# Kernel tuning notes

Measured on AMD Instinct MI355X. Metric: run time of the kernel, lower is better.

Reference implementation:

```python
import jax, jax.numpy as jnp
import numpy as np

THETA = 10000.0


def _apply_rope(xh, positions, theta):
    # xh: [B, H, S, d_k]; positions: [S] int
    d_k = xh.shape[-1]
    inv_freq = theta ** (-jnp.arange(0, d_k, 2, dtype=jnp.float32) / d_k)  # [d_k/2]
    angles = positions.astype(jnp.float32)[:, None] * inv_freq[None, :]     # [S, d_k/2]
    cos = jnp.cos(angles)
    sin = jnp.sin(angles)
    x1 = xh[..., 0::2]
    x2 = xh[..., 1::2]
    r1 = x1 * cos - x2 * sin
    r2 = x1 * sin + x2 * cos
    return jnp.stack([r1, r2], axis=-1).reshape(xh.shape)


def setup_inputs() -> dict:
    key = jax.random.key(0)
    ks = jax.random.split(key, 5)
    B, S, D = 2, 2048, 1024
    std = np.sqrt(1.0 / D).astype(np.float32)
    return {
        "x": jax.random.normal(ks[0], (B, S, D), dtype=jnp.float32),
        "token_positions": jnp.arange(S, dtype=jnp.int64 if jax.config.jax_enable_x64 else jnp.int32),
        "Wq": jax.random.normal(ks[1], (D, D), dtype=jnp.float32) * std,
        "Wk": jax.random.normal(ks[2], (D, D), dtype=jnp.float32) * std,
        "Wv": jax.random.normal(ks[3], (D, D), dtype=jnp.float32) * std,
        "Wo": jax.random.normal(ks[4], (D, D), dtype=jnp.float32) * std,
    }


def reference(x, token_positions, Wq, Wk, Wv, Wo):
    B, S, D = x.shape
    n_heads = 16
    d_k = D // n_heads

    # QKV projections (torch does x @ W.T)
    q = x @ Wq.T
    k = x @ Wk.T
    v = x @ Wv.T

    def split_heads(t):  # [B,S,D] -> [B,H,S,d_k]
        return t.reshape(B, S, n_heads, d_k).transpose(0, 2, 1, 3)

    qh = _apply_rope(split_heads(q), token_positions, THETA)
    kh = _apply_rope(split_heads(k), token_positions, THETA)
    vh = split_heads(v)

    scores = jnp.einsum("bhqd,bhkd->bhqk", qh, kh) / jnp.sqrt(jnp.float32(d_k))
    causal = jnp.tril(jnp.ones((S, S), dtype=bool))
    scores = jnp.where(causal, scores, -jnp.inf)
    attn = jax.nn.softmax(scores, axis=-1)

    out_h = jnp.einsum("bhqk,bhkd->bhqd", attn, vh)  # [B,H,S,d_k]
    out = out_h.transpose(0, 2, 1, 3).reshape(B, S, D)
    return out @ Wo.T
```

## Files before the change

### kernel.cpp

```cpp
#include <hip/hip_runtime.h>

typedef unsigned int u32;
typedef __attribute__((ext_vector_type(8))) short short8;
typedef __attribute__((ext_vector_type(4))) float f32x4;

__device__ __forceinline__ unsigned short f2bf(float f) {
  union { float f; u32 u; } x; x.f = f;
  u32 u = x.u;
  return (unsigned short)((u + 0x7fffu + ((u >> 16) & 1u)) >> 16);
}
__device__ __forceinline__ float bf2f(unsigned short b) {
  union { u32 u; float f; } x; x.u = ((u32)b) << 16;
  return x.f;
}
__device__ __forceinline__ f32x4 mfma_bf16(short8 a, short8 b, f32x4 c) {
  return __builtin_amdgcn_mfma_f32_16x16x32_bf16(a, b, c, 0, 0, 0);
}

typedef __attribute__((address_space(3))) unsigned int lds_u32;
typedef const __attribute__((address_space(1))) unsigned int glb_u32;
__device__ __forceinline__ void gload_lds16(const unsigned short* g, unsigned short* l) {
  __builtin_amdgcn_global_load_lds((glb_u32*)g, (lds_u32*)l, 16, 0, 0);
}

__global__ __launch_bounds__(256) void cvt_kernel(const float* __restrict__ src,
                                                  unsigned short* __restrict__ dst, int n4) {
  int i = blockIdx.x * 256 + threadIdx.x;
  if (i >= n4) return;
  float4 v = ((const float4*)src)[i];
  ushort4 o;
  o.x = f2bf(v.x); o.y = f2bf(v.y); o.z = f2bf(v.z); o.w = f2bf(v.w);
  ((ushort4*)dst)[i] = o;
}

__global__ __launch_bounds__(256) void cvt_w_kernel(const float* __restrict__ wq,
                                                    const float* __restrict__ wk,
                                                    const float* __restrict__ wv,
                                                    const float* __restrict__ wo,
                                                    unsigned short* __restrict__ dqkv,
                                                    unsigned short* __restrict__ dwo) {
  const int i = blockIdx.x * 256 + threadIdx.x;
  const int w = blockIdx.y;
  const float* src = (w == 0) ? wq : (w == 1) ? wk : (w == 2) ? wv : wo;
  unsigned short* dst = (w == 3) ? dwo : dqkv + (size_t)w * 1048576;
  float4 v = ((const float4*)src)[i];
  ushort4 o;
  o.x = f2bf(v.x); o.y = f2bf(v.y); o.z = f2bf(v.z); o.w = f2bf(v.w);
  ((ushort4*)dst)[i] = o;
}

__global__ __launch_bounds__(256) void gemm_qkv(const unsigned short* __restrict__ A,
                                                const unsigned short* __restrict__ B,
                                                unsigned short* __restrict__ qk,
                                                unsigned short* __restrict__ kk,
                                                unsigned short* __restrict__ vtm) {
  constexpr int K = 1024;
  __shared__ unsigned short As[128 * 32];
  __shared__ unsigned short Bs[128 * 32];
  const int tid = threadIdx.x;
  const int wave = tid >> 6, lane = tid & 63;
  const int l15 = lane & 15, quad = lane >> 4;
  const int wr = wave >> 1, wc = wave & 1;
  const int m0 = blockIdx.y * 128, n0 = blockIdx.x * 128;
  f32x4 acc[4][4] = {};
  const int srow = wave * 32 + (lane >> 2);
  const int scol = (lane & 3) * 8;
  const unsigned short* Ag0 = A + (size_t)(m0 + srow) * K + scol;
  const unsigned short* Ag1 = A + (size_t)(m0 + srow + 16) * K + scol;
  const unsigned short* Bg0 = B + (size_t)(n0 + srow) * K + scol;
  const unsigned short* Bg1 = B + (size_t)(n0 + srow + 16) * K + scol;
  unsigned short* Al0 = &As[wave * 1024];
  unsigned short* Al1 = &As[wave * 1024 + 512];
  unsigned short* Bl0 = &Bs[wave * 1024];
  unsigned short* Bl1 = &Bs[wave * 1024 + 512];
  for (int k0 = 0; k0 < K; k0 += 32) {
    __syncthreads();
    gload_lds16(Ag0 + k0, Al0);
    gload_lds16(Ag1 + k0, Al1);
    gload_lds16(Bg0 + k0, Bl0);
    gload_lds16(Bg1 + k0, Bl1);
    __syncthreads();
    short8 a[4], b[4];
#pragma unroll
    for (int i = 0; i < 4; ++i) a[i] = *(const short8*)&As[(wr * 64 + i * 16 + l15) * 32 + quad * 8];
#pragma unroll
    for (int j = 0; j < 4; ++j) b[j] = *(const short8*)&Bs[(wc * 64 + j * 16 + l15) * 32 + quad * 8];
#pragma unroll
    for (int i = 0; i < 4; ++i)
#pragma unroll
      for (int j = 0; j < 4; ++j) acc[i][j] = mfma_bf16(a[i], b[j], acc[i][j]);
  }
  const int proj = n0 >> 10;
  const int nn0 = (n0 & 1023) + wc * 64;
  if (proj < 2) {
    unsigned short* dst = (proj == 0) ? qk : kk;
#pragma unroll
    for (int i = 0; i < 4; ++i) {
      const int mb = m0 + wr * 64 + i * 16 + quad * 4;
#pragma unroll
      for (int j = 0; j < 4; ++j) {
        const int nn = nn0 + j * 16 + l15;
#pragma unroll
        for (int r = 0; r < 4; ++r) dst[(size_t)(mb + r) * 1024 + nn] = f2bf(acc[i][j][r]);
      }
    }
  } else {
#pragma unroll
    for (int i = 0; i < 4; ++i) {
      const int mb = m0 + wr * 64 + i * 16 + quad * 4;
      const int bb = mb >> 11, s = mb & 2047;
#pragma unroll
      for (int j = 0; j < 4; ++j) {
        const int nn = nn0 + j * 16 + l15;
        const int h = nn >> 6, d = nn & 63;
        ushort4 v4;
        v4.x = f2bf(acc[i][j][0]); v4.y = f2bf(acc[i][j][1]);
        v4.z = f2bf(acc[i][j][2]); v4.w = f2bf(acc[i][j][3]);
        *(ushort4*)&vtm[(((size_t)bb * 16 + h) * 64 + d) * 2048 + s] = v4;
      }
    }
  }
}

__global__ __launch_bounds__(256) void rope_kernel(unsigned short* __restrict__ q,
                                                   unsigned short* __restrict__ k,
                                                   const int* __restrict__ pos) {
  const int idx = blockIdx.x * 256 + threadIdx.x;
  const int i = idx & 31;
  const int h = (idx >> 5) & 15;
  const int s = (idx >> 9) & 2047;
  const int b = idx >> 20;
  const float p = (float)pos[s];
  const float inv = exp2f(-0.4152410118609203f * (float)i);
  float sn, cs;
  sincosf(p * inv, &sn, &cs);
  const size_t base = ((size_t)(b * 2048 + s)) * 1024 + h * 64 + 2 * i;
  {
    u32* qp = (u32*)(q + base);
    u32 w = *qp;
    float x1 = bf2f((unsigned short)(w & 0xffff)), x2 = bf2f((unsigned short)(w >> 16));
    *qp = (u32)f2bf(x1 * cs - x2 * sn) | ((u32)f2bf(x1 * sn + x2 * cs) << 16);
  }
  {
    u32* kp = (u32*)(k + base);
    u32 w = *kp;
    float x1 = bf2f((unsigned short)(w & 0xffff)), x2 = bf2f((unsigned short)(w >> 16));
    *kp = (u32)f2bf(x1 * cs - x2 * sn) | ((u32)f2bf(x1 * sn + x2 * cs) << 16);
  }
}

__global__ __launch_bounds__(256) void attn_shared(const unsigned short* __restrict__ qk,
                                                   const unsigned short* __restrict__ kk,
                                                   const unsigned short* __restrict__ vtm,
                                                   unsigned short* __restrict__ om) {
  __shared__ unsigned short Ks[64 * 64];
  __shared__ unsigned short Vs[64 * 64];
  __shared__ u32 PTb[4][2][16 * 36];
  const int tid = threadIdx.x;
  const int wave = tid >> 6, lane = tid & 63;
  const int l15 = lane & 15, quad = lane >> 4;
  u32* PT0 = &PTb[wave][0][0];
  u32* PT1 = &PTb[wave][1][0];
  const int bid = blockIdx.x;
  const int bh = bid & 31;
  const int qblk = 15 - (bid >> 5);
  const int b = bh >> 4, h = bh & 15;
  const int qbase = qblk * 128 + wave * 32;
  const unsigned short* Qp = qk + (size_t)b * 2048 * 1024 + h * 64;
  const unsigned short* Kp = kk + (size_t)b * 2048 * 1024 + h * 64;
  const unsigned short* Vp = vtm + (size_t)bh * 64 * 2048;
  short8 qf[2][2];
#pragma unroll
  for (int f = 0; f < 2; ++f)
#pragma unroll
    for (int hh = 0; hh < 2; ++hh)
      qf[f][hh] = *(const short8*)(Qp + (size_t)(qbase + f * 16 + l15) * 1024 + hh * 32 + quad * 8);
  f32x4 o4[2][4] = {};
  f32x4 ls[2] = {};
  short8 ones;
#pragma unroll
  for (int j = 0; j < 8; ++j) ones[j] = (short)0x3F80;
  const float SC = 0.18033688011112042f;
  const int nkb = (qblk * 128 + 191) >> 6;
  const int nkw = (qbase + 95) >> 6;
  const int srow = wave * 16 + (lane >> 3);
  const int scs = (((lane & 7) ^ (srow & 7)) * 8);
  const unsigned short* KgB = Kp + (size_t)srow * 1024 + scs;
  const unsigned short* VgB = Vp + (size_t)srow * 2048 + scs;
  unsigned short* Kl0 = &Ks[(wave * 16) * 64];
  unsigned short* Kl1 = &Ks[(wave * 16 + 8) * 64];
  unsigned short* Vl0 = &Vs[(wave * 16) * 64];
  unsigned short* Vl1 = &Vs[(wave * 16 + 8) * 64];
  const int sw0 = ((quad ^ (l15 & 7)) * 8);
  const int sw1 = (((4 + quad) ^ (l15 & 7)) * 8);
  for (int kt = 0; kt < nkb; ++kt) {
    const int kbase = kt << 6;
    __syncthreads();
    gload_lds16(KgB + (size_t)kbase * 1024, Kl0);
    gload_lds16(KgB + (size_t)kbase * 1024 + 8 * 1024, Kl1);
    gload_lds16(VgB + kbase, Vl0);
    gload_lds16(VgB + kbase + 8 * 2048, Vl1);
    __syncthreads();
    if (kt < nkw) {
      short8 kb[4][2], vb[4][2];
#pragma unroll
      for (int nt = 0; nt < 4; ++nt) {
        kb[nt][0] = *(const short8*)&Ks[(nt * 16 + l15) * 64 + sw0];
        kb[nt][1] = *(const short8*)&Ks[(nt * 16 + l15) * 64 + sw1];
      }
#pragma unroll
      for (int t = 0; t < 4; ++t) {
        vb[t][0] = *(const short8*)&Vs[(t * 16 + l15) * 64 + sw0];
        vb[t][1] = *(const short8*)&Vs[(t * 16 + l15) * 64 + sw1];
      }
      f32x4 s4[2][4] = {};
#pragma unroll
      for (int f = 0; f < 2; ++f)
#pragma unroll
        for (int nt = 0; nt < 4; ++nt) {
          s4[f][nt] = mfma_bf16(kb[nt][0], qf[f][0], s4[f][nt]);
          s4[f][nt] = mfma_bf16(kb[nt][1], qf[f][1], s4[f][nt]);
        }
      const bool edge = (kbase + 63 > qbase);
#pragma unroll
      for (int f = 0; f < 2; ++f) {
        const int qrow = qbase + f * 16 + l15;
        u32* PTf = f ? PT1 : PT0;
#pragma unroll
        for (int nt = 0; nt < 4; ++nt) {
          const int kv0 = kbase + nt * 16 + quad * 4;
          float p0 = exp2f(s4[f][nt][0] * SC);
          float p1 = exp2f(s4[f][nt][1] * SC);
          float p2 = exp2f(s4[f][nt][2] * SC);
          float p3 = exp2f(s4[f][nt][3] * SC);
          if (edge) {
            if (kv0 > qrow) p0 = 0.f;
            if (kv0 + 1 > qrow) p1 = 0.f;
            if (kv0 + 2 > qrow) p2 = 0.f;
            if (kv0 + 3 > qrow) p3 = 0.f;
          }
          uint2 w;
          w.x = (u32)f2bf(p0) | ((u32)f2bf(p1) << 16);
          w.y = (u32)f2bf(p2) | ((u32)f2bf(p3) << 16);
          *(uint2*)&PTf[l15 * 36 + nt * 8 + quad * 2] = w;
        }
      }
      short8 pa[2][2];
#pragma unroll
      for (int f = 0; f < 2; ++f) {
        const u32* PTf = f ? PT1 : PT0;
#pragma unroll
        for (int hh = 0; hh < 2; ++hh)
          pa[f][hh] = *(const short8*)&PTf[l15 * 36 + hh * 16 + quad * 4];
      }
#pragma unroll
      for (int f = 0; f < 2; ++f) {
#pragma unroll
        for (int t = 0; t < 4; ++t) {
          o4[f][t] = mfma_bf16(pa[f][0], vb[t][0], o4[f][t]);
          o4[f][t] = mfma_bf16(pa[f][1], vb[t][1], o4[f][t]);
        }
        ls[f] = mfma_bf16(pa[f][0], ones, ls[f]);
        ls[f] = mfma_bf16(pa[f][1], ones, ls[f]);
      }
    }
  }
#pragma unroll
  for (int f = 0; f < 2; ++f) {
    f32x4 rl;
#pragma unroll
    for (int r = 0; r < 4; ++r) rl[r] = 1.f / ls[f][r];
#pragma unroll
    for (int t = 0; t < 4; ++t)
#pragma unroll
      for (int r = 0; r < 4; ++r) {
        const int srw = qbase + f * 16 + quad * 4 + r;
        om[((size_t)b * 2048 + srw) * 1024 + h * 64 + t * 16 + l15] = f2bf(o4[f][t][r] * rl[r]);
      }
  }
}

__global__ __launch_bounds__(256) void gemm_out(const unsigned short* __restrict__ A,
                                                const unsigned short* __restrict__ B,
                                                float* __restrict__ C) {
  constexpr int K = 1024;
  __shared__ unsigned short As[64 * 32];
  __shared__ unsigned short Bs[128 * 32];
  const int tid = threadIdx.x;
  const int wave = tid >> 6, lane = tid & 63;
  const int l15 = lane & 15, quad = lane >> 4;
  const int m0 = blockIdx.y * 64, n0 = blockIdx.x * 128;
  f32x4 acc[4][2] = {};
  const int lr = lane >> 2, lc = (lane & 3) * 8;
  const unsigned short* Ag  = A + (size_t)(m0 + wave * 16 + lr) * K + lc;
  const unsigned short* Bg0 = B + (size_t)(n0 + wave * 32 + lr) * K + lc;
  const unsigned short* Bg1 = B + (size_t)(n0 + wave * 32 + 16 + lr) * K + lc;
  unsigned short* Al  = &As[wave * 512];
  unsigned short* Bl0 = &Bs[wave * 1024];
  unsigned short* Bl1 = &Bs[wave * 1024 + 512];
  for (int k0 = 0; k0 < K; k0 += 32) {
    __syncthreads();
    gload_lds16(Ag + k0, Al);
    gload_lds16(Bg0 + k0, Bl0);
    gload_lds16(Bg1 + k0, Bl1);
    __syncthreads();
    short8 a[4], b[2];
#pragma unroll
    for (int i = 0; i < 4; ++i) a[i] = *(const short8*)&As[(i * 16 + l15) * 32 + quad * 8];
#pragma unroll
    for (int j = 0; j < 2; ++j) b[j] = *(const short8*)&Bs[(wave * 32 + j * 16 + l15) * 32 + quad * 8];
#pragma unroll
    for (int i = 0; i < 4; ++i)
#pragma unroll
      for (int j = 0; j < 2; ++j) acc[i][j] = mfma_bf16(a[i], b[j], acc[i][j]);
  }
#pragma unroll
  for (int i = 0; i < 4; ++i)
#pragma unroll
    for (int j = 0; j < 2; ++j)
#pragma unroll
      for (int r = 0; r < 4; ++r)
        C[(size_t)(m0 + i * 16 + quad * 4 + r) * 1024 + n0 + wave * 32 + j * 16 + l15] =
            acc[i][j][r];
}

extern "C" void kernel_launch(void* const* d_in, const int* in_sizes, int n_in,
                              void* d_out, int out_size, void* d_ws, size_t ws_size,
                              hipStream_t stream) {
  const float* x  = (const float*)d_in[0];
  const int* pos  = (const int*)d_in[1];
  const float* Wq = (const float*)d_in[2];
  const float* Wk = (const float*)d_in[3];
  const float* Wv = (const float*)d_in[4];
  const float* Wo = (const float*)d_in[5];
  float* out = (float*)d_out;
  char* ws = (char*)d_ws;
  unsigned short* xb   = (unsigned short*)(ws);
  unsigned short* wqkv = (unsigned short*)(ws + (size_t)( 8 << 20));
  unsigned short* wob  = (unsigned short*)(ws + (size_t)(14 << 20));
  unsigned short* qkb  = (unsigned short*)(ws + (size_t)(16 << 20));
  unsigned short* kkb  = (unsigned short*)(ws + (size_t)(24 << 20));
  unsigned short* vtm  = (unsigned short*)(ws + (size_t)(32 << 20));
  unsigned short* om   = (unsigned short*)(ws + (size_t)(40 << 20));

  const int NX4 = 4096 * 1024 / 4;
  hipLaunchKernelGGL(cvt_kernel, dim3(NX4 / 256), dim3(256), 0, stream, x, xb, NX4);
  hipLaunchKernelGGL(cvt_w_kernel, dim3(1024, 4), dim3(256), 0, stream, Wq, Wk, Wv, Wo, wqkv, wob);

  hipLaunchKernelGGL(gemm_qkv, dim3(24, 32), dim3(256), 0, stream, xb, wqkv, qkb, kkb, vtm);
  hipLaunchKernelGGL(rope_kernel, dim3(8192), dim3(256), 0, stream, qkb, kkb, pos);
  hipLaunchKernelGGL(attn_shared, dim3(512), dim3(256), 0, stream, qkb, kkb, vtm, om);
  hipLaunchKernelGGL(gemm_out, dim3(8, 64), dim3(256), 0, stream, om, wob, out);
}
```

Measured before the change: 229.2 us.

## Double GEMM K-tile to 64 with XOR-swizzled LDS layout

Both the QKV and output projection GEMMs now stage 64-wide K slices instead of 32, which halves the number of barrier pairs per K loop. The shared-memory layout uses an XOR swizzle on 16-byte chunks so the fragment reads avoid LDS bank conflicts on the longer rows. In exchange, LDS use per block doubles, which may reduce occupancy, and each thread issues more loads per step.

```diff
diff --git a/kernel.cpp b/kernel.cpp
--- a/kernel.cpp
+++ b/kernel.cpp
@@ -55,40 +55,48 @@
                                                 unsigned short* __restrict__ kk,
                                                 unsigned short* __restrict__ vtm) {
   constexpr int K = 1024;
-  __shared__ unsigned short As[128 * 32];
-  __shared__ unsigned short Bs[128 * 32];
+  __shared__ unsigned short As[128 * 64];
+  __shared__ unsigned short Bs[128 * 64];
   const int tid = threadIdx.x;
   const int wave = tid >> 6, lane = tid & 63;
   const int l15 = lane & 15, quad = lane >> 4;
   const int wr = wave >> 1, wc = wave & 1;
   const int m0 = blockIdx.y * 128, n0 = blockIdx.x * 128;
   f32x4 acc[4][4] = {};
-  const int srow = wave * 32 + (lane >> 2);
-  const int scol = (lane & 3) * 8;
-  const unsigned short* Ag0 = A + (size_t)(m0 + srow) * K + scol;
-  const unsigned short* Ag1 = A + (size_t)(m0 + srow + 16) * K + scol;
-  const unsigned short* Bg0 = B + (size_t)(n0 + srow) * K + scol;
-  const unsigned short* Bg1 = B + (size_t)(n0 + srow + 16) * K + scol;
-  unsigned short* Al0 = &As[wave * 1024];
-  unsigned short* Al1 = &As[wave * 1024 + 512];
-  unsigned short* Bl0 = &Bs[wave * 1024];
-  unsigned short* Bl1 = &Bs[wave * 1024 + 512];
-  for (int k0 = 0; k0 < K; k0 += 32) {
-    __syncthreads();
-    gload_lds16(Ag0 + k0, Al0);
-    gload_lds16(Ag1 + k0, Al1);
-    gload_lds16(Bg0 + k0, Bl0);
-    gload_lds16(Bg1 + k0, Bl1);
-    __syncthreads();
-    short8 a[4], b[4];
-#pragma unroll
-    for (int i = 0; i < 4; ++i) a[i] = *(const short8*)&As[(wr * 64 + i * 16 + l15) * 32 + quad * 8];
-#pragma unroll
-    for (int j = 0; j < 4; ++j) b[j] = *(const short8*)&Bs[(wc * 64 + j * 16 + l15) * 32 + quad * 8];
+  const int srow = wave * 32 + (lane >> 3);
+  const int scol = (((lane & 7) ^ ((lane >> 3) & 7)) * 8);
+  const unsigned short* Ag = A + (size_t)(m0 + srow) * K + scol;
+  const unsigned short* Bg = B + (size_t)(n0 + srow) * K + scol;
+  const int sw0 = ((0 + quad) ^ (l15 & 7)) * 8;
+  const int sw1 = ((4 + quad) ^ (l15 & 7)) * 8;
+  for (int k0 = 0; k0 < K; k0 += 64) {
+    __syncthreads();
+#pragma unroll
+    for (int r = 0; r < 4; ++r) {
+      gload_lds16(Ag + k0 + (size_t)(8 * r) * K, &As[(wave * 32 + 8 * r) * 64]);
+      gload_lds16(Bg + k0 + (size_t)(8 * r) * K, &Bs[(wave * 32 + 8 * r) * 64]);
+    }
+    __syncthreads();
+    short8 a[4][2], b[4][2];
+#pragma unroll
+    for (int i = 0; i < 4; ++i) {
+      const int row = (wr * 64 + i * 16 + l15) * 64;
+      a[i][0] = *(const short8*)&As[row + sw0];
+      a[i][1] = *(const short8*)&As[row + sw1];
+    }
+#pragma unroll
+    for (int j = 0; j < 4; ++j) {
+      const int row = (wc * 64 + j * 16 + l15) * 64;
+      b[j][0] = *(const short8*)&Bs[row + sw0];
+      b[j][1] = *(const short8*)&Bs[row + sw1];
+    }
 #pragma unroll
     for (int i = 0; i < 4; ++i)
 #pragma unroll
-      for (int j = 0; j < 4; ++j) acc[i][j] = mfma_bf16(a[i], b[j], acc[i][j]);
+      for (int j = 0; j < 4; ++j) {
+        acc[i][j] = mfma_bf16(a[i][0], b[j][0], acc[i][j]);
+        acc[i][j] = mfma_bf16(a[i][1], b[j][1], acc[i][j]);
+      }
   }
   const int proj = n0 >> 10;
   const int nn0 = (n0 & 1023) + wc * 64;
@@ -284,35 +292,47 @@
                                                 const unsigned short* __restrict__ B,
                                                 float* __restrict__ C) {
   constexpr int K = 1024;
-  __shared__ unsigned short As[64 * 32];
-  __shared__ unsigned short Bs[128 * 32];
+  __shared__ unsigned short As[64 * 64];
+  __shared__ unsigned short Bs[128 * 64];
   const int tid = threadIdx.x;
   const int wave = tid >> 6, lane = tid & 63;
   const int l15 = lane & 15, quad = lane >> 4;
   const int m0 = blockIdx.y * 64, n0 = blockIdx.x * 128;
   f32x4 acc[4][2] = {};
-  const int lr = lane >> 2, lc = (lane & 3) * 8;
-  const unsigned short* Ag  = A + (size_t)(m0 + wave * 16 + lr) * K + lc;
-  const unsigned short* Bg0 = B + (size_t)(n0 + wave * 32 + lr) * K + lc;
-  const unsigned short* Bg1 = B + (size_t)(n0 + wave * 32 + 16 + lr) * K + lc;
-  unsigned short* Al  = &As[wave * 512];
-  unsigned short* Bl0 = &Bs[wave * 1024];
-  unsigned short* Bl1 = &Bs[wave * 1024 + 512];
-  for (int k0 = 0; k0 < K; k0 += 32) {
-    __syncthreads();
-    gload_lds16(Ag + k0, Al);
-    gload_lds16(Bg0 + k0, Bl0);
-    gload_lds16(Bg1 + k0, Bl1);
-    __syncthreads();
-    short8 a[4], b[2];
-#pragma unroll
-    for (int i = 0; i < 4; ++i) a[i] = *(const short8*)&As[(i * 16 + l15) * 32 + quad * 8];
-#pragma unroll
-    for (int j = 0; j < 2; ++j) b[j] = *(const short8*)&Bs[(wave * 32 + j * 16 + l15) * 32 + quad * 8];
+  const int lr = lane >> 3;
+  const int scol = (((lane & 7) ^ (lr & 7)) * 8);
+  const unsigned short* Ag = A + (size_t)(m0 + wave * 16 + lr) * K + scol;
+  const unsigned short* Bg = B + (size_t)(n0 + wave * 32 + lr) * K + scol;
+  const int sw0 = ((0 + quad) ^ (l15 & 7)) * 8;
+  const int sw1 = ((4 + quad) ^ (l15 & 7)) * 8;
+  for (int k0 = 0; k0 < K; k0 += 64) {
+    __syncthreads();
+    gload_lds16(Ag + k0, &As[(wave * 16) * 64]);
+    gload_lds16(Ag + k0 + (size_t)8 * K, &As[(wave * 16 + 8) * 64]);
+#pragma unroll
+    for (int r = 0; r < 4; ++r)
+      gload_lds16(Bg + k0 + (size_t)(8 * r) * K, &Bs[(wave * 32 + 8 * r) * 64]);
+    __syncthreads();
+    short8 a[4][2], b[2][2];
+#pragma unroll
+    for (int i = 0; i < 4; ++i) {
+      const int row = (i * 16 + l15) * 64;
+      a[i][0] = *(const short8*)&As[row + sw0];
+      a[i][1] = *(const short8*)&As[row + sw1];
+    }
+#pragma unroll
+    for (int j = 0; j < 2; ++j) {
+      const int row = (wave * 32 + j * 16 + l15) * 64;
+      b[j][0] = *(const short8*)&Bs[row + sw0];
+      b[j][1] = *(const short8*)&Bs[row + sw1];
+    }
 #pragma unroll
     for (int i = 0; i < 4; ++i)
 #pragma unroll
-      for (int j = 0; j < 2; ++j) acc[i][j] = mfma_bf16(a[i], b[j], acc[i][j]);
+      for (int j = 0; j < 2; ++j) {
+        acc[i][j] = mfma_bf16(a[i][0], b[j][0], acc[i][j]);
+        acc[i][j] = mfma_bf16(a[i][1], b[j][1], acc[i][j]);
+      }
   }
 #pragma unroll
   for (int i = 0; i < 4; ++i)
```

New measurement: 216.3 us. 1.06x faster.
